# Optimization experiments

Hardware: AMD Instinct MI355X
Metric: run time of the kernel (lower is better)

The kernel has to match this reference:

```python
import jax, jax.numpy as jnp
import numpy as np

B, L, E, H, D, OUT = 4, 2048, 1024, 8, 128, 1024


def setup_inputs() -> dict:
    key = jax.random.key(0)
    ks = jax.random.split(key, 6)
    stdv = 1.0 / np.sqrt(D)
    return {
        "k": jax.random.normal(ks[0], (B, L, E), dtype=jnp.float32),
        "q": jax.random.normal(ks[1], (B, L, E), dtype=jnp.float32),
        "w_kx": jax.random.uniform(ks[2], (H, E, D), minval=-stdv, maxval=stdv, dtype=jnp.float32),
        "w_qx": jax.random.uniform(ks[3], (H, E, D), minval=-stdv, maxval=stdv, dtype=jnp.float32),
        "proj_w": jax.random.normal(ks[4], (OUT, H * D), dtype=jnp.float32) * 0.02,
        "proj_b": jnp.zeros((OUT,), dtype=jnp.float32),
        "flag": False,
    }


def reference(k, q, w_kx, w_qx, proj_w, proj_b, flag):
    # Per-head sigmoid projections, vectorized over heads (original loops over heads).
    d = w_kx.shape[-1]
    kx = jax.nn.sigmoid(jnp.einsum('ble,hed->bhld', k, w_kx))  # [B,H,Lk,D]
    if flag:
        # flag==True: q is used directly (already hidden_dim-sized), shared across heads
        qx = jnp.broadcast_to(q[:, None], (q.shape[0], kx.shape[1], q.shape[1], q.shape[2]))
    else:
        qx = jax.nn.sigmoid(jnp.einsum('bqe,hed->bhqd', q, w_qx))  # [B,H,Lq,D]
    # scaled dot-product score + softmax over key axis
    score = jnp.einsum('bhqd,bhkd->bhqk', qx, kx) * (1.0 / jnp.sqrt(jnp.asarray(d, kx.dtype)))
    attn = jax.nn.softmax(score, axis=-1)
    out = jnp.einsum('bhqk,bhkd->bhqd', attn, kx)  # [B,H,Lq,D]
    # concat heads along feature dim, then linear projection (dropout p=0 -> identity)
    b, h, lq, _ = out.shape
    out = out.transpose(0, 2, 1, 3).reshape(b, lq, h * d)
    return out @ proj_w.T + proj_b
```

## Files before the change

### kernel.cpp

```cpp
#include <hip/hip_runtime.h>

#define BB 4
#define LL 2048
#define EE 1024
#define HH 8
#define DD 128
#define OO 1024
#define MM (BB*LL)
#define ND (HH*DD)

#define QBLK 128
#define KVBLK 64
#define NT (LL / KVBLK)

#define C2 0.12751920678739807f

typedef __bf16 bf16;
typedef unsigned short u16;
typedef __bf16 bf16x8 __attribute__((ext_vector_type(8)));
typedef __bf16 bf16x4 __attribute__((ext_vector_type(4)));
typedef float  f32x4  __attribute__((ext_vector_type(4)));

__device__ __forceinline__ void gl16(const bf16* g, bf16* l) {
#if __has_builtin(__builtin_amdgcn_global_load_lds)
    __builtin_amdgcn_global_load_lds((const __attribute__((address_space(1))) char*)g,
                                     (__attribute__((address_space(3))) char*)l, 16, 0, 0);
#else
    *(bf16x8*)l = *(const bf16x8*)g;
#endif
}

__device__ __forceinline__ float fexp2(float x) {
#if __has_builtin(__builtin_amdgcn_exp2f)
    return __builtin_amdgcn_exp2f(x);
#else
    return exp2f(x);
#endif
}

__device__ __forceinline__ bf16x8 cvt8p(float4 f0, float4 f1) {
    bf16x8 v;
    v[0] = (bf16)f0.x; v[1] = (bf16)f0.y; v[2] = (bf16)f0.z; v[3] = (bf16)f0.w;
    v[4] = (bf16)f1.x; v[5] = (bf16)f1.y; v[6] = (bf16)f1.z; v[7] = (bf16)f1.w;
    return v;
}

__global__ void detect_kernel(const u16* __restrict__ data, int* __restrict__ mode) {
    const int l = threadIdx.x;
    int cnt = 0;
#pragma unroll
    for (int i = 0; i < 8; i++) {
        int e = (data[l * 8 + i] >> 7) & 0xFF;
        cnt += (e >= 117 && e <= 132) ? 1 : 0;
    }
    cnt += __shfl_xor(cnt, 1);
    cnt += __shfl_xor(cnt, 2);
    cnt += __shfl_xor(cnt, 4);
    cnt += __shfl_xor(cnt, 8);
    cnt += __shfl_xor(cnt, 16);
    cnt += __shfl_xor(cnt, 32);
    if (l == 0) *mode = (cnt > 400) ? 1 : 0;
}

__global__ __launch_bounds__(256) void fill_kernel(float* __restrict__ out, float v, int n) {
    int i = blockIdx.x * 256 + threadIdx.x;
    if (i < n) out[i] = v;
}

__global__ __launch_bounds__(256) void wtrans_kernel(const void* __restrict__ in0,
                                                     const void* __restrict__ in1,
                                                     bf16* __restrict__ outT0,
                                                     bf16* __restrict__ outT1,
                                                     const int* __restrict__ mode) {
    const void* in = blockIdx.y ? in1 : in0;
    bf16* outT = blockIdx.y ? outT1 : outT0;
    int idx = blockIdx.x * 256 + threadIdx.x;
    int i4 = idx * 4;
    int h = i4 >> 17;
    int rem = i4 & 131071;
    int e = rem >> 7;
    int d = rem & 127;
    size_t ob = ((size_t)h * DD + d) * EE + e;
    if (*mode) {
        bf16x4 v = *(const bf16x4*)((const bf16*)in + i4);
        outT[ob]          = v[0];
        outT[ob + EE]     = v[1];
        outT[ob + 2 * EE] = v[2];
        outT[ob + 3 * EE] = v[3];
    } else {
        float4 v = *(const float4*)((const float*)in + i4);
        outT[ob]          = (bf16)v.x;
        outT[ob + EE]     = (bf16)v.y;
        outT[ob + 2 * EE] = (bf16)v.z;
        outT[ob + 3 * EE] = (bf16)v.w;
    }
}

__global__ __launch_bounds__(256) void gemm_kernel(const void* __restrict__ A0,
                                                   const void* __restrict__ A1,
                                                   const void* __restrict__ BT0,
                                                   const void* __restrict__ BT1,
                                                   bf16* __restrict__ outBF0,
                                                   bf16* __restrict__ outBF1,
                                                   bf16* __restrict__ outT,
                                                   float* __restrict__ outF,
                                                   const void* __restrict__ PB,
                                                   const int* __restrict__ mode,
                                                   const int epi) {
    __shared__ __align__(16) bf16 As[128 * 64];
    __shared__ __align__(16) bf16 Bs[128 * 64];
    const int md = *mode;
    const int t = threadIdx.x;
    const int w = t >> 6, l = t & 63;
    const int lr = l & 15, lg = l >> 4;
    const int wr = w >> 1, wc = w & 1;
    const int o = blockIdx.x + (blockIdx.y << 3);
    const int half = (epi == 3) ? (o >> 9) : 0;
    const int oo = o & 511;
    const int mt = (oo & 7) * 8 + ((oo >> 3) & 7);
    const int ntile = oo >> 6;
    const int m0 = mt * 128, n0 = ntile * 128;
    const void* A = half ? A1 : A0;
    const void* BT = half ? BT1 : BT0;

    const int useF = (md == 0);
    const float* fS = (const float*)((epi == 3) ? A : BT);
    bf16* fDst = (epi == 3) ? As : Bs;
    const int f0 = (epi == 3) ? m0 : n0;
    const bf16* gS = (const bf16*)((epi == 3) ? BT : A);
    bf16* gDst = (epi == 3) ? Bs : As;
    const int g0 = (epi == 3) ? n0 : m0;

    f32x4 acc[4][4];
    const f32x4 zero = {0.f, 0.f, 0.f, 0.f};
#pragma unroll
    for (int i = 0; i < 4; i++)
#pragma unroll
        for (int j = 0; j < 4; j++) acc[i][j] = zero;

    float4 rS[4][2];
    if (useF) {
#pragma unroll
        for (int p = 0; p < 4; p++) {
            const int id = p * 256 + t;
            const int row = id >> 3, cc = id & 7;
            const float* src = fS + (size_t)(f0 + row) * 1024 + cc * 8;
            rS[p][0] = *(const float4*)src;
            rS[p][1] = *(const float4*)(src + 4);
        }
    }

    for (int kt = 0; kt < 16; ++kt) {
        const int k0 = kt * 64;
        __syncthreads();
        if (useF) {
#pragma unroll
            for (int p = 0; p < 4; p++) {
                const int id = p * 256 + t;
                const int row = id >> 3, cc = id & 7;
                *(bf16x8*)(fDst + row * 64 + ((cc ^ (row & 7)) << 3)) = cvt8p(rS[p][0], rS[p][1]);
            }
#pragma unroll
            for (int p = 0; p < 4; p++) {
                const int id = p * 256 + t;
                const int row = id >> 3;
                const int c = (id & 7) ^ (row & 7);
                gl16(gS + (size_t)(g0 + row) * 1024 + k0 + c * 8, gDst + (p * 256 + w * 64) * 8);
            }
        } else {
#pragma unroll
            for (int p = 0; p < 4; p++) {
                const int id = p * 256 + t;
                const int row = id >> 3;
                const int c = (id & 7) ^ (row & 7);
                gl16((const bf16*)A + (size_t)(m0 + row) * 1024 + k0 + c * 8,
                     As + (p * 256 + w * 64) * 8);
                gl16((const bf16*)BT + (size_t)(n0 + row) * 1024 + k0 + c * 8,
                     Bs + (p * 256 + w * 64) * 8);
            }
        }
        __syncthreads();
        if (useF && kt + 1 < 16) {
            const int k0n = k0 + 64;
#pragma unroll
            for (int p = 0; p < 4; p++) {
                const int id = p * 256 + t;
                const int row = id >> 3, cc = id & 7;
                const float* src = fS + (size_t)(f0 + row) * 1024 + k0n + cc * 8;
                rS[p][0] = *(const float4*)src;
                rS[p][1] = *(const float4*)(src + 4);
            }
        }
        bf16x8 af[4][2], bg[4][2];
#pragma unroll
        for (int i = 0; i < 4; i++) {
            const int ar = wr * 64 + i * 16 + lr;
#pragma unroll
            for (int ks = 0; ks < 2; ks++)
                af[i][ks] = *(const bf16x8*)(As + ar * 64 + (((ks * 4 + lg) ^ (ar & 7)) << 3));
        }
#pragma unroll
        for (int j = 0; j < 4; j++) {
            const int br = wc * 64 + j * 16 + lr;
#pragma unroll
            for (int ks = 0; ks < 2; ks++)
                bg[j][ks] = *(const bf16x8*)(Bs + br * 64 + (((ks * 4 + lg) ^ (br & 7)) << 3));
        }
#pragma unroll
        for (int i = 0; i < 4; i++)
#pragma unroll
            for (int j = 0; j < 4; j++) {
                acc[i][j] = __builtin_amdgcn_mfma_f32_16x16x32_bf16(af[i][0], bg[j][0], acc[i][j], 0, 0, 0);
                acc[i][j] = __builtin_amdgcn_mfma_f32_16x16x32_bf16(af[i][1], bg[j][1], acc[i][j], 0, 0, 0);
            }
    }

    if (epi == 3) {
        bf16* outBF = half ? outBF1 : outBF0;
        const float mulf = half ? C2 : 1.0f;
        const int b_idx = m0 >> 11;
        const int h = n0 >> 7;
#pragma unroll
        for (int i = 0; i < 4; i++) {
#pragma unroll
            for (int j = 0; j < 4; j++) {
                const int gr = m0 + wr * 64 + i * 16 + lg * 4;
                const int gc = n0 + wc * 64 + j * 16 + lr;
                float s0 = mulf / (1.0f + __expf(-acc[i][j][0]));
                float s1 = mulf / (1.0f + __expf(-acc[i][j][1]));
                float s2 = mulf / (1.0f + __expf(-acc[i][j][2]));
                float s3 = mulf / (1.0f + __expf(-acc[i][j][3]));
                outBF[(size_t)gr * ND + gc]           = (bf16)s0;
                outBF[(size_t)(gr + 1) * ND + gc]     = (bf16)s1;
                outBF[(size_t)(gr + 2) * ND + gc]     = (bf16)s2;
                outBF[(size_t)(gr + 3) * ND + gc]     = (bf16)s3;
                if (!half) {
                    bf16x4 pk;
                    pk[0] = (bf16)s0; pk[1] = (bf16)s1; pk[2] = (bf16)s2; pk[3] = (bf16)s3;
                    const int d = gc & 127;
                    const int lrow = gr & 2047;
                    *(bf16x4*)(outT + (((size_t)(h * BB + b_idx)) * DD + d) * LL + lrow) = pk;
                }
            }
        }
    } else {
#pragma unroll
        for (int j = 0; j < 4; j++) {
            const int gc = n0 + wc * 64 + j * 16 + lr;
            const float bias = md ? (float)((const bf16*)PB)[gc] : ((const float*)PB)[gc];
#pragma unroll
            for (int i = 0; i < 4; i++) {
                const int gr = m0 + wr * 64 + i * 16 + lg * 4;
#pragma unroll
                for (int reg = 0; reg < 4; reg++)
                    outF[(size_t)(gr + reg) * OO + gc] = acc[i][j][reg] + bias;
            }
        }
    }
}

__global__ __launch_bounds__(512, 4) void attn_kernel(const bf16* __restrict__ QX,
                                                      const bf16* __restrict__ KX,
                                                      const bf16* __restrict__ KXT,
                                                      bf16* __restrict__ AO) {
    __shared__ __align__(16) bf16 Kl[2][KVBLK * 128];
    __shared__ __align__(16) bf16 Vt[2][128 * KVBLK];
    __shared__ __align__(16) bf16 Pl[8][16 * 64];
    const int t = threadIdx.x;
    const int w = t >> 6, l = t & 63;
    const int lr = l & 15, lg = l >> 4;
    const int bid = blockIdx.x;
    const int orig = (bid & 7) * 64 + (bid >> 3);
    const int bh = orig >> 4;
    const int h = bh & 7, b = bh >> 3;
    const int q0 = (orig & 15) * QBLK;
    const bf16* qxh = QX + (size_t)(b * LL) * ND + h * DD;
    const bf16* kxh = KX + (size_t)(b * LL) * ND + h * DD;
    const bf16* kxt = KXT + ((size_t)(h * BB + b)) * DD * LL;

    const int kid1 = 512 + t;
    const int krow0 = t >> 4,    kcd0 = t & 15;
    const int krow1 = kid1 >> 4, kcd1 = kid1 & 15;
    const int vrow0 = t >> 3,    vcd0 = t & 7;
    const int vrow1 = kid1 >> 3, vcd1 = kid1 & 7;
    const bf16* kps0 = kxh + (size_t)krow0 * ND + (kcd0 ^ (krow0 & 15)) * 8;
    const bf16* kps1 = kxh + (size_t)krow1 * ND + (kcd1 ^ (krow1 & 15)) * 8;
    const bf16* vps0 = kxt + (size_t)vrow0 * LL + (vcd0 ^ (vrow0 & 7)) * 8;
    const bf16* vps1 = kxt + (size_t)vrow1 * LL + (vcd1 ^ (vrow1 & 7)) * 8;

    bf16x8 qf[4];
    const int qrow = q0 + w * 16 + lr;
#pragma unroll
    for (int s = 0; s < 4; s++)
        qf[s] = *(const bf16x8*)(qxh + (size_t)qrow * ND + s * 32 + lg * 8);

    gl16(kps0, Kl[0] + t * 8);
    gl16(kps1, Kl[0] + kid1 * 8);
    gl16(vps0, Vt[0] + t * 8);
    gl16(vps1, Vt[0] + kid1 * 8);
    __syncthreads();

    f32x4 oacc[8];
    const f32x4 zero = {0.f, 0.f, 0.f, 0.f};
#pragma unroll
    for (int n = 0; n < 8; n++) oacc[n] = zero;
    float psum = 0.f;

    for (int kt = 0; kt < NT; ++kt) {
        const int cur = kt & 1;
        if (kt + 1 < NT) {
            const size_t ko = (size_t)(kt + 1) * KVBLK * ND;
            const int vo = (kt + 1) * KVBLK;
            gl16(kps0 + ko, Kl[cur ^ 1] + t * 8);
            gl16(kps1 + ko, Kl[cur ^ 1] + kid1 * 8);
            gl16(vps0 + vo, Vt[cur ^ 1] + t * 8);
            gl16(vps1 + vo, Vt[cur ^ 1] + kid1 * 8);
        }
        const bf16* KlC = Kl[cur];
        const bf16* VtC = Vt[cur];

        f32x4 sa[4];
        __builtin_amdgcn_s_setprio(1);
#pragma unroll
        for (int n = 0; n < 2; n++) {
            sa[n] = zero;
#pragma unroll
            for (int ks = 0; ks < 4; ks++) {
                int arow = n * 16 + lr;
                bf16x8 kb = *(const bf16x8*)(KlC + arow * 128 + ((((ks * 4 + lg) ^ (arow & 15))) << 3));
                sa[n] = __builtin_amdgcn_mfma_f32_16x16x32_bf16(kb, qf[ks], sa[n], 0, 0, 0);
            }
        }
        __builtin_amdgcn_s_setprio(0);
#pragma unroll
        for (int n = 0; n < 2; n++) {
            bf16x4 pk;
#pragma unroll
            for (int j = 0; j < 4; j++) {
                float p = fexp2(sa[n][j]);
                psum += p;
                pk[j] = (bf16)p;
            }
            const int chunk = (2 * n + (lg >> 1)) ^ (lr & 7);
            *(bf16x4*)(Pl[w] + lr * 64 + chunk * 8 + (lg & 1) * 4) = pk;
        }
        __builtin_amdgcn_s_setprio(1);
#pragma unroll
        for (int n = 2; n < 4; n++) {
            sa[n] = zero;
#pragma unroll
            for (int ks = 0; ks < 4; ks++) {
                int arow = n * 16 + lr;
                bf16x8 kb = *(const bf16x8*)(KlC + arow * 128 + ((((ks * 4 + lg) ^ (arow & 15))) << 3));
                sa[n] = __builtin_amdgcn_mfma_f32_16x16x32_bf16(kb, qf[ks], sa[n], 0, 0, 0);
            }
        }
        __builtin_amdgcn_s_setprio(0);
#pragma unroll
        for (int n = 2; n < 4; n++) {
            bf16x4 pk;
#pragma unroll
            for (int j = 0; j < 4; j++) {
                float p = fexp2(sa[n][j]);
                psum += p;
                pk[j] = (bf16)p;
            }
            const int chunk = (2 * n + (lg >> 1)) ^ (lr & 7);
            *(bf16x4*)(Pl[w] + lr * 64 + chunk * 8 + (lg & 1) * 4) = pk;
        }
        asm volatile("s_waitcnt lgkmcnt(0)" ::: "memory");
        __builtin_amdgcn_sched_barrier(0);
        bf16x8 pb0 = *(const bf16x8*)(Pl[w] + lr * 64 + (((lg ^ (lr & 7))) << 3));
        bf16x8 pb1 = *(const bf16x8*)(Pl[w] + lr * 64 + ((((4 + lg) ^ (lr & 7))) << 3));
        __builtin_amdgcn_s_setprio(1);
#pragma unroll
        for (int n = 0; n < 8; n++) {
            int vrow = n * 16 + lr;
            bf16x8 vb0 = *(const bf16x8*)(VtC + vrow * 64 + (((lg ^ (vrow & 7))) << 3));
            oacc[n] = __builtin_amdgcn_mfma_f32_16x16x32_bf16(vb0, pb0, oacc[n], 0, 0, 0);
            bf16x8 vb1 = *(const bf16x8*)(VtC + vrow * 64 + ((((4 + lg) ^ (vrow & 7))) << 3));
            oacc[n] = __builtin_amdgcn_mfma_f32_16x16x32_bf16(vb1, pb1, oacc[n], 0, 0, 0);
        }
        __builtin_amdgcn_s_setprio(0);
        __syncthreads();
    }
    float tot = psum;
    tot += __shfl_xor(tot, 16);
    tot += __shfl_xor(tot, 32);
    const float linv = 1.0f / tot;
    const int arow = b * LL + q0 + w * 16 + lr;
    bf16* aoRow = AO + (size_t)arow * ND + h * DD;
#pragma unroll
    for (int n = 0; n < 8; n++) {
        bf16x4 o;
#pragma unroll
        for (int reg = 0; reg < 4; reg++) o[reg] = (bf16)(oacc[n][reg] * linv);
        *(bf16x4*)(aoRow + n * 16 + lg * 4) = o;
    }
}

extern "C" void kernel_launch(void* const* d_in, const int* in_sizes, int n_in,
                              void* d_out, int out_size, void* d_ws, size_t ws_size,
                              hipStream_t stream) {
    (void)in_sizes; (void)n_in;
    float* out = (float*)d_out;

    const size_t NEED = ((size_t)(2 + 2 + 16 + 16 + 16 + 16) << 20) + 256;
    if (ws_size < NEED) {
        hipLaunchKernelGGL(fill_kernel, dim3((out_size + 255) / 256), dim3(256), 0, stream,
                           out, (float)(ws_size >> 20), out_size);
        return;
    }

    int* mode = (int*)d_ws;
    bf16* base = (bf16*)((char*)d_ws + 256);
    bf16* wkT = base;
    bf16* wqT = wkT + (size_t)HH * DD * EE;
    bf16* kx  = wqT + (size_t)HH * DD * EE;
    bf16* qx  = kx  + (size_t)MM * ND;
    bf16* kxT = qx  + (size_t)MM * ND;
    bf16* ao  = kxT + (size_t)HH * MM * DD;

    hipLaunchKernelGGL(detect_kernel, dim3(1), dim3(64), 0, stream, (const u16*)d_in[0], mode);
    hipLaunchKernelGGL(wtrans_kernel, dim3(HH * EE * DD / 4 / 256, 2), dim3(256), 0, stream,
                       d_in[2], d_in[3], wkT, wqT, mode);
    hipLaunchKernelGGL(gemm_kernel, dim3(8, 128), dim3(256), 0, stream,
                       d_in[0], d_in[1], wkT, wqT, kx, qx, kxT,
                       (float*)nullptr, (const void*)nullptr, mode, 3);
    hipLaunchKernelGGL(attn_kernel, dim3(512), dim3(512), 0, stream, qx, kx, kxT, ao);
    hipLaunchKernelGGL(gemm_kernel, dim3(8, 64), dim3(256), 0, stream,
                       ao, (const void*)nullptr, d_in[4], (const void*)nullptr,
                       (bf16*)nullptr, (bf16*)nullptr, (bf16*)nullptr, out, d_in[5], mode, 2);
}
```

Before: 170.0 us.

## Double-buffer LDS tiles in projection GEMM to overlap loads with MFMA

The GEMM kernel's shared-memory A/B tiles become two-stage ping-pong buffers. The next K tile is written or async-loaded into the alternate buffer while MFMAs consume the current one, which cuts the loop from two barriers per iteration to one. Float source prefetch now runs two tiles ahead. LDS use doubles to 64KB per block and launch_bounds requests 2 blocks per CU, which may cap registers or occupancy.

```diff
diff --git a/kernel.cpp b/kernel.cpp
--- a/kernel.cpp
+++ b/kernel.cpp
@@ -96,19 +96,19 @@
     }
 }
 
-__global__ __launch_bounds__(256) void gemm_kernel(const void* __restrict__ A0,
-                                                   const void* __restrict__ A1,
-                                                   const void* __restrict__ BT0,
-                                                   const void* __restrict__ BT1,
-                                                   bf16* __restrict__ outBF0,
-                                                   bf16* __restrict__ outBF1,
-                                                   bf16* __restrict__ outT,
-                                                   float* __restrict__ outF,
-                                                   const void* __restrict__ PB,
-                                                   const int* __restrict__ mode,
-                                                   const int epi) {
-    __shared__ __align__(16) bf16 As[128 * 64];
-    __shared__ __align__(16) bf16 Bs[128 * 64];
+__global__ __launch_bounds__(256, 2) void gemm_kernel(const void* __restrict__ A0,
+                                                      const void* __restrict__ A1,
+                                                      const void* __restrict__ BT0,
+                                                      const void* __restrict__ BT1,
+                                                      bf16* __restrict__ outBF0,
+                                                      bf16* __restrict__ outBF1,
+                                                      bf16* __restrict__ outT,
+                                                      float* __restrict__ outF,
+                                                      const void* __restrict__ PB,
+                                                      const int* __restrict__ mode,
+                                                      const int epi) {
+    __shared__ __align__(16) bf16 As[2][128 * 64];
+    __shared__ __align__(16) bf16 Bs[2][128 * 64];
     const int md = *mode;
     const int t = threadIdx.x;
     const int w = t >> 6, l = t & 63;
@@ -124,12 +124,11 @@
     const void* BT = half ? BT1 : BT0;
 
     const int useF = (md == 0);
-    const float* fS = (const float*)((epi == 3) ? A : BT);
-    bf16* fDst = (epi == 3) ? As : Bs;
-    const int f0 = (epi == 3) ? m0 : n0;
-    const bf16* gS = (const bf16*)((epi == 3) ? BT : A);
-    bf16* gDst = (epi == 3) ? Bs : As;
-    const int g0 = (epi == 3) ? n0 : m0;
+    const int fIsA = (epi == 3);
+    const float* fS = (const float*)(fIsA ? A : BT);
+    const int f0 = fIsA ? m0 : n0;
+    const bf16* gS = (const bf16*)(fIsA ? BT : A);
+    const int g0 = fIsA ? n0 : m0;
 
     f32x4 acc[4][4];
     const f32x4 zero = {0.f, 0.f, 0.f, 0.f};
@@ -139,6 +138,7 @@
         for (int j = 0; j < 4; j++) acc[i][j] = zero;
 
     float4 rS[4][2];
+
     if (useF) {
 #pragma unroll
         for (int p = 0; p < 4; p++) {
@@ -148,47 +148,85 @@
             rS[p][0] = *(const float4*)src;
             rS[p][1] = *(const float4*)(src + 4);
         }
-    }
+        bf16* fD = fIsA ? As[0] : Bs[0];
+#pragma unroll
+        for (int p = 0; p < 4; p++) {
+            const int id = p * 256 + t;
+            const int row = id >> 3, cc = id & 7;
+            *(bf16x8*)(fD + row * 64 + ((cc ^ (row & 7)) << 3)) = cvt8p(rS[p][0], rS[p][1]);
+        }
+        bf16* gD = fIsA ? Bs[0] : As[0];
+#pragma unroll
+        for (int p = 0; p < 4; p++) {
+            const int id = p * 256 + t;
+            const int row = id >> 3;
+            const int c = (id & 7) ^ (row & 7);
+            gl16(gS + (size_t)(g0 + row) * 1024 + c * 8, gD + (p * 256 + w * 64) * 8);
+        }
+#pragma unroll
+        for (int p = 0; p < 4; p++) {
+            const int id = p * 256 + t;
+            const int row = id >> 3, cc = id & 7;
+            const float* src = fS + (size_t)(f0 + row) * 1024 + 64 + cc * 8;
+            rS[p][0] = *(const float4*)src;
+            rS[p][1] = *(const float4*)(src + 4);
+        }
+    } else {
+#pragma unroll
+        for (int p = 0; p < 4; p++) {
+            const int id = p * 256 + t;
+            const int row = id >> 3;
+            const int c = (id & 7) ^ (row & 7);
+            gl16((const bf16*)A + (size_t)(m0 + row) * 1024 + c * 8,
+                 As[0] + (p * 256 + w * 64) * 8);
+            gl16((const bf16*)BT + (size_t)(n0 + row) * 1024 + c * 8,
+                 Bs[0] + (p * 256 + w * 64) * 8);
+        }
+    }
+    __syncthreads();
 
     for (int kt = 0; kt < 16; ++kt) {
-        const int k0 = kt * 64;
-        __syncthreads();
-        if (useF) {
-#pragma unroll
-            for (int p = 0; p < 4; p++) {
-                const int id = p * 256 + t;
-                const int row = id >> 3, cc = id & 7;
-                *(bf16x8*)(fDst + row * 64 + ((cc ^ (row & 7)) << 3)) = cvt8p(rS[p][0], rS[p][1]);
-            }
-#pragma unroll
-            for (int p = 0; p < 4; p++) {
-                const int id = p * 256 + t;
-                const int row = id >> 3;
-                const int c = (id & 7) ^ (row & 7);
-                gl16(gS + (size_t)(g0 + row) * 1024 + k0 + c * 8, gDst + (p * 256 + w * 64) * 8);
-            }
-        } else {
-#pragma unroll
-            for (int p = 0; p < 4; p++) {
-                const int id = p * 256 + t;
-                const int row = id >> 3;
-                const int c = (id & 7) ^ (row & 7);
-                gl16((const bf16*)A + (size_t)(m0 + row) * 1024 + k0 + c * 8,
-                     As + (p * 256 + w * 64) * 8);
-                gl16((const bf16*)BT + (size_t)(n0 + row) * 1024 + k0 + c * 8,
-                     Bs + (p * 256 + w * 64) * 8);
-            }
-        }
-        __syncthreads();
-        if (useF && kt + 1 < 16) {
-            const int k0n = k0 + 64;
-#pragma unroll
-            for (int p = 0; p < 4; p++) {
-                const int id = p * 256 + t;
-                const int row = id >> 3, cc = id & 7;
-                const float* src = fS + (size_t)(f0 + row) * 1024 + k0n + cc * 8;
-                rS[p][0] = *(const float4*)src;
-                rS[p][1] = *(const float4*)(src + 4);
+        const int cur = kt & 1, alt = cur ^ 1;
+        if (kt + 1 < 16) {
+            const int k0n = (kt + 1) * 64;
+            if (useF) {
+                bf16* fD = fIsA ? As[alt] : Bs[alt];
+#pragma unroll
+                for (int p = 0; p < 4; p++) {
+                    const int id = p * 256 + t;
+                    const int row = id >> 3, cc = id & 7;
+                    *(bf16x8*)(fD + row * 64 + ((cc ^ (row & 7)) << 3)) = cvt8p(rS[p][0], rS[p][1]);
+                }
+                bf16* gD = fIsA ? Bs[alt] : As[alt];
+#pragma unroll
+                for (int p = 0; p < 4; p++) {
+                    const int id = p * 256 + t;
+                    const int row = id >> 3;
+                    const int c = (id & 7) ^ (row & 7);
+                    gl16(gS + (size_t)(g0 + row) * 1024 + k0n + c * 8, gD + (p * 256 + w * 64) * 8);
+                }
+                if (kt + 2 < 16) {
+                    const int k0p = (kt + 2) * 64;
+#pragma unroll
+                    for (int p = 0; p < 4; p++) {
+                        const int id = p * 256 + t;
+                        const int row = id >> 3, cc = id & 7;
+                        const float* src = fS + (size_t)(f0 + row) * 1024 + k0p + cc * 8;
+                        rS[p][0] = *(const float4*)src;
+                        rS[p][1] = *(const float4*)(src + 4);
+                    }
+                }
+            } else {
+#pragma unroll
+                for (int p = 0; p < 4; p++) {
+                    const int id = p * 256 + t;
+                    const int row = id >> 3;
+                    const int c = (id & 7) ^ (row & 7);
+                    gl16((const bf16*)A + (size_t)(m0 + row) * 1024 + k0n + c * 8,
+                         As[alt] + (p * 256 + w * 64) * 8);
+                    gl16((const bf16*)BT + (size_t)(n0 + row) * 1024 + k0n + c * 8,
+                         Bs[alt] + (p * 256 + w * 64) * 8);
+                }
             }
         }
         bf16x8 af[4][2], bg[4][2];
@@ -197,14 +235,14 @@
             const int ar = wr * 64 + i * 16 + lr;
 #pragma unroll
             for (int ks = 0; ks < 2; ks++)
-                af[i][ks] = *(const bf16x8*)(As + ar * 64 + (((ks * 4 + lg) ^ (ar & 7)) << 3));
+                af[i][ks] = *(const bf16x8*)(As[cur] + ar * 64 + (((ks * 4 + lg) ^ (ar & 7)) << 3));
         }
 #pragma unroll
         for (int j = 0; j < 4; j++) {
             const int br = wc * 64 + j * 16 + lr;
 #pragma unroll
             for (int ks = 0; ks < 2; ks++)
-                bg[j][ks] = *(const bf16x8*)(Bs + br * 64 + (((ks * 4 + lg) ^ (br & 7)) << 3));
+                bg[j][ks] = *(const bf16x8*)(Bs[cur] + br * 64 + (((ks * 4 + lg) ^ (br & 7)) << 3));
         }
 #pragma unroll
         for (int i = 0; i < 4; i++)
@@ -213,6 +251,7 @@
                 acc[i][j] = __builtin_amdgcn_mfma_f32_16x16x32_bf16(af[i][0], bg[j][0], acc[i][j], 0, 0, 0);
                 acc[i][j] = __builtin_amdgcn_mfma_f32_16x16x32_bf16(af[i][1], bg[j][1], acc[i][j], 0, 0, 0);
             }
+        __syncthreads();
     }
 
     if (epi == 3) {
```

Result: no change. 173.3 us (+1.9%).
